# Optimization experiments

Hardware: AMD Instinct MI355X
Metric: run time of the kernel (lower is better)

Reference implementation:

```python
import jax, jax.numpy as jnp
import numpy as np

N_HEAD = 16
D_MODEL = 2048

def setup_inputs() -> dict:
    key = jax.random.key(0)
    ks = jax.random.split(key, 9)
    B, T, C = 2, 2048, D_MODEL
    s = 1.0 / np.sqrt(C)
    return {
        "idx": jax.random.normal(ks[0], (B, T, C), dtype=jnp.float32),
        "Wq": jax.random.normal(ks[1], (C, C), dtype=jnp.float32) * s,
        "bq": jnp.zeros((C,), dtype=jnp.float32),
        "Wk": jax.random.normal(ks[2], (C, C), dtype=jnp.float32) * s,
        "bk": jnp.zeros((C,), dtype=jnp.float32),
        "Wv": jax.random.normal(ks[3], (C, C), dtype=jnp.float32) * s,
        "bv": jnp.zeros((C,), dtype=jnp.float32),
        "Wo": jax.random.normal(ks[4], (C, C), dtype=jnp.float32) * s,
        "bo": jnp.zeros((C,), dtype=jnp.float32),
    }

def reference(idx, Wq, bq, Wk, bk, Wv, bv, Wo, bo):
    B, T, C = idx.shape
    hs = C // N_HEAD
    def split_heads(x):
        return x.reshape(B, T, N_HEAD, hs).transpose(0, 2, 1, 3)  # [B,H,T,hs]
    q = split_heads(idx @ Wq + bq)
    k = split_heads(idx @ Wk + bk)
    v = split_heads(idx @ Wv + bv)
    scale = 1.0 / jnp.sqrt(jnp.asarray(hs, dtype=idx.dtype))
    scores = jnp.einsum('bhqd,bhkd->bhqk', q, k) * scale
    causal = jnp.tril(jnp.ones((T, T), dtype=bool))
    scores = jnp.where(causal, scores, -jnp.inf)
    attn = jax.nn.softmax(scores, axis=-1)
    out = jnp.einsum('bhqk,bhkd->bhqd', attn, v)
    out = out.transpose(0, 2, 1, 3).reshape(B, T, C)
    return out @ Wo + bo
```

## Files before the change

### kernel.cpp

```cpp
#include <hip/hip_runtime.h>
#include <hip/hip_bf16.h>

#define TT 2048
#define CC 2048
#define HH 16
#define HS 128
#define BB 2
#define MM (BB*TT)

typedef __attribute__((ext_vector_type(8))) short bf16x8;
typedef __attribute__((ext_vector_type(4))) short bf16x4;
typedef __attribute__((ext_vector_type(4))) float f32x4;
typedef __attribute__((ext_vector_type(16))) float f32x16;

__device__ __forceinline__ short f2bf(float x) {
    unsigned u = __float_as_uint(x);
    unsigned r = (u + 0x7FFFu + ((u >> 16) & 1u)) >> 16;
    return (short)r;
}

__device__ __forceinline__ void gl_lds16(const void* g, void* l) {
    __builtin_amdgcn_global_load_lds(
        (const __attribute__((address_space(1))) unsigned int*)g,
        (__attribute__((address_space(3))) unsigned int*)l,
        16, 0, 0);
}

__global__ void cvt_bf16_kernel(const float* __restrict__ x, short* __restrict__ y, int n) {
    int stride = gridDim.x * blockDim.x;
    for (int i = blockIdx.x * blockDim.x + threadIdx.x; i < n/4; i += stride) {
        float4 v = reinterpret_cast<const float4*>(x)[i];
        bf16x4 s;
        s[0] = f2bf(v.x); s[1] = f2bf(v.y); s[2] = f2bf(v.z); s[3] = f2bf(v.w);
        reinterpret_cast<bf16x4*>(y)[i] = s;
    }
}

__global__ void wt_kernel(const float* __restrict__ w0, const float* __restrict__ w1,
                          const float* __restrict__ w2, const float* __restrict__ w3,
                          short* __restrict__ o0, short* __restrict__ o1,
                          short* __restrict__ o2, short* __restrict__ o3)
{
    const float* W; short* Wt;
    switch (blockIdx.z) {
        case 0:  W = w0; Wt = o0; break;
        case 1:  W = w1; Wt = o1; break;
        case 2:  W = w2; Wt = o2; break;
        default: W = w3; Wt = o3; break;
    }
    __shared__ float tile[32][33];
    int tx = threadIdx.x, ty = threadIdx.y;
    int k0 = blockIdx.x * 32, n0 = blockIdx.y * 32;
    #pragma unroll
    for (int i = 0; i < 4; ++i)
        tile[ty + i*8][tx] = W[(size_t)(k0 + ty + i*8) * CC + n0 + tx];
    __syncthreads();
    #pragma unroll
    for (int i = 0; i < 4; ++i)
        Wt[(size_t)(n0 + ty + i*8) * CC + k0 + tx] = f2bf(tile[tx][ty + i*8]);
}

template<int MODE>
__launch_bounds__(256)
__global__ void gemm_bt_kernel(const short* __restrict__ A, const short* __restrict__ Bt,
                               const float* __restrict__ bias, void* __restrict__ dst,
                               float scale)
{
    __shared__ __align__(16) short As[128*64];
    __shared__ __align__(16) short Bs[128*64];
    const int tid = threadIdx.x;
    const int lane = tid & 63;
    const int g = lane >> 4, fr = lane & 15;
    const int wid = tid >> 6;
    const int wr = wid >> 1, wc = wid & 1;
    const int m0 = blockIdx.x * 128, n0 = blockIdx.y * 128;

    f32x4 acc[4][4];
    #pragma unroll
    for (int i = 0; i < 4; ++i)
        #pragma unroll
        for (int j = 0; j < 4; ++j) acc[i][j] = (f32x4){0.f,0.f,0.f,0.f};

    for (int k0 = 0; k0 < CC; k0 += 64) {
        __syncthreads();
        #pragma unroll
        for (int i = 0; i < 4; ++i) {
            int c = i*256 + tid;
            int row = c >> 3;
            int kbl = ((c & 7) * 16) ^ ((row & 7) << 4);
            gl_lds16(reinterpret_cast<const char*>(A) + ((size_t)(m0+row)*CC + k0)*2 + kbl,
                     reinterpret_cast<char*>(As) + c*16);
        }
        #pragma unroll
        for (int i = 0; i < 4; ++i) {
            int c = i*256 + tid;
            int row = c >> 3;
            int kbl = ((c & 7) * 16) ^ ((row & 7) << 4);
            gl_lds16(reinterpret_cast<const char*>(Bt) + ((size_t)(n0+row)*CC + k0)*2 + kbl,
                     reinterpret_cast<char*>(Bs) + c*16);
        }
        __syncthreads();
        #pragma unroll
        for (int cch = 0; cch < 2; ++cch) {
            bf16x8 a[4], b[4];
            #pragma unroll
            for (int i = 0; i < 4; ++i) {
                int row = wr*64 + i*16 + fr;
                int kph = (cch*64 + g*16) ^ ((row & 7) << 4);
                a[i] = *reinterpret_cast<const bf16x8*>(
                    reinterpret_cast<const char*>(As) + row*128 + kph);
            }
            #pragma unroll
            for (int j = 0; j < 4; ++j) {
                int row = wc*64 + j*16 + fr;
                int kph = (cch*64 + g*16) ^ ((row & 7) << 4);
                b[j] = *reinterpret_cast<const bf16x8*>(
                    reinterpret_cast<const char*>(Bs) + row*128 + kph);
            }
            #pragma unroll
            for (int i = 0; i < 4; ++i)
                #pragma unroll
                for (int j = 0; j < 4; ++j)
                    acc[i][j] = __builtin_amdgcn_mfma_f32_16x16x32_bf16(a[i], b[j], acc[i][j], 0, 0, 0);
        }
    }

    #pragma unroll
    for (int j = 0; j < 4; ++j) {
        int n = n0 + wc*64 + j*16 + fr;
        float bv = bias[n];
        #pragma unroll
        for (int i = 0; i < 4; ++i) {
            #pragma unroll
            for (int r = 0; r < 4; ++r) {
                int m = m0 + wr*64 + i*16 + g*4 + r;
                float val = (acc[i][j][r] + bv) * scale;
                if (MODE == 0) {
                    int bb = m >> 11, t = m & (TT-1);
                    int h  = n >> 7,  d = n & (HS-1);
                    reinterpret_cast<short*>(dst)[((size_t)(bb*HH + h)*TT + t)*HS + d] = f2bf(val);
                } else if (MODE == 2) {
                    int bb = m >> 11, t = m & (TT-1);
                    int h  = n >> 7,  d = n & (HS-1);
                    reinterpret_cast<short*>(dst)[((size_t)(bb*HH + h)*HS + d)*TT + t] = f2bf(val);
                } else {
                    reinterpret_cast<float*>(dst)[(size_t)m*CC + n] = val;
                }
            }
        }
    }
}

__launch_bounds__(256, 2)
__global__ void attn_kernel(const short* __restrict__ Q, const short* __restrict__ K,
                            const short* __restrict__ Vt, short* __restrict__ O)
{
    __shared__ __align__(16) short Ks[2][64*128];
    __shared__ __align__(16) short Vs[2][128*64];

    const int tid = threadIdx.x;
    const int lane = tid & 63;
    const int wid = tid >> 6;
    const int l5 = lane >> 5;
    const int q31 = lane & 31;
    const bool hif = (l5 != 0);

    const int dd = blockIdx.x;
    const int g8 = dd & 7;
    const int s  = (dd >> 3) & 31;
    const int half = dd >> 8;
    const int bh = g8*4 + (s >> 3);
    const int u  = s & 7;
    const int qb = half ? u : (15 - u);
    const int q0 = qb * 128;
    const int wq0 = q0 + wid*32;

    const short* Qh = Q + (size_t)bh * TT * HS;
    const char*  Kg = (const char*)(K  + (size_t)bh * TT * HS);
    const char*  Vg = (const char*)(Vt + (size_t)bh * HS * TT);

    bf16x8 qf[8];
    #pragma unroll
    for (int dk = 0; dk < 8; ++dk)
        qf[dk] = *reinterpret_cast<const bf16x8*>(
            Qh + (size_t)(wq0 + q31)*HS + dk*16 + l5*8);

    f32x16 o[4];
    #pragma unroll
    for (int c = 0; c < 4; ++c)
        #pragma unroll
        for (int r = 0; r < 16; ++r) o[c][r] = 0.f;
    float mrun = -1e30f, lrun = 0.f;

    auto stage = [&](int kv0, int p) {
        char* Kd = reinterpret_cast<char*>(Ks[p]);
        char* Vd = reinterpret_cast<char*>(Vs[p]);
        #pragma unroll
        for (int i = 0; i < 4; ++i) {
            int c = i*256 + tid;
            int row = c >> 4;
            int lg  = ((c & 15) * 16) ^ ((row & 7) << 4);
            gl_lds16(Kg + (size_t)(kv0 + row)*256 + lg, Kd + c*16);
        }
        #pragma unroll
        for (int i = 0; i < 4; ++i) {
            int c = i*256 + tid;
            int row = c >> 3;
            int lg  = ((c & 7) * 16) ^ ((row & 7) << 4);
            gl_lds16(Vg + ((size_t)row*TT + kv0)*2 + lg, Vd + c*16);
        }
    };

    const int nst = q0/64 + 2;
    stage(0, 0);

    for (int t = 0; t < nst; ++t) {
        const int kv0 = t * 64;
        __syncthreads();
        if (t + 1 < nst) stage(kv0 + 64, (t+1) & 1);

        if (kv0 > wq0 + 31) continue;

        const char* Kl = reinterpret_cast<const char*>(Ks[t & 1]);
        const char* Vl = reinterpret_cast<const char*>(Vs[t & 1]);

        f32x16 st[2];
        #pragma unroll
        for (int t2 = 0; t2 < 2; ++t2)
            #pragma unroll
            for (int r = 0; r < 16; ++r) st[t2][r] = 0.f;
        #pragma unroll
        for (int t2 = 0; t2 < 2; ++t2) {
            int krow = t2*32 + q31;
            int rsw = (krow & 7) << 4;
            #pragma unroll
            for (int dk = 0; dk < 8; ++dk) {
                bf16x8 kf = *reinterpret_cast<const bf16x8*>(
                    Kl + krow*256 + ((dk*32 + l5*16) ^ rsw));
                st[t2] = __builtin_amdgcn_mfma_f32_32x32x16_bf16(kf, qf[dk], st[t2], 0, 0, 0);
            }
        }
        if (kv0 + 63 > wq0) {
            int qrow = wq0 + q31;
            #pragma unroll
            for (int t2 = 0; t2 < 2; ++t2)
                #pragma unroll
                for (int r = 0; r < 16; ++r) {
                    int kv = kv0 + t2*32 + (r & 3) + ((r >> 2) << 3) + l5*4;
                    if (kv > qrow) st[t2][r] = -1e30f;
                }
        }
        float pm = -1e30f;
        #pragma unroll
        for (int t2 = 0; t2 < 2; ++t2)
            #pragma unroll
            for (int r = 0; r < 16; ++r) pm = fmaxf(pm, st[t2][r]);
        if (__any(pm > mrun + 8.f)) {
            float pmf = fmaxf(pm, __shfl_xor(pm, 32));
            float mn = fmaxf(mrun, pmf);
            float al = __builtin_amdgcn_exp2f(mrun - mn);
            mrun = mn; lrun *= al;
            #pragma unroll
            for (int c = 0; c < 4; ++c)
                #pragma unroll
                for (int r = 0; r < 16; ++r) o[c][r] *= al;
        }
        float ps = 0.f;
        #pragma unroll
        for (int t2 = 0; t2 < 2; ++t2)
            #pragma unroll
            for (int r = 0; r < 16; ++r) {
                float pv = __builtin_amdgcn_exp2f(st[t2][r] - mrun);
                st[t2][r] = pv;
                ps += pv;
            }
        lrun += ps;
        unsigned pw[2][8];
        #pragma unroll
        for (int t2 = 0; t2 < 2; ++t2)
            #pragma unroll
            for (int w = 0; w < 8; ++w)
                asm("v_cvt_pk_bf16_f32 %0, %1, %2"
                    : "=v"(pw[t2][w]) : "v"(st[t2][2*w]), "v"(st[t2][2*w+1]));
        #pragma unroll
        for (int c4 = 0; c4 < 4; ++c4) {
            int t2 = c4 >> 1, b0 = (c4 & 1) * 4;
            unsigned A0 = pw[t2][b0+0], A1 = pw[t2][b0+1];
            unsigned A2 = pw[t2][b0+2], A3 = pw[t2][b0+3];
            unsigned X0 = (unsigned)__shfl_xor((int)A0, 32);
            unsigned X1 = (unsigned)__shfl_xor((int)A1, 32);
            unsigned X2 = (unsigned)__shfl_xor((int)A2, 32);
            unsigned X3 = (unsigned)__shfl_xor((int)A3, 32);
            union { unsigned u[4]; bf16x8 v; } fu;
            fu.u[0] = hif ? X2 : A0;
            fu.u[1] = hif ? X3 : A1;
            fu.u[2] = hif ? A2 : X0;
            fu.u[3] = hif ? A3 : X1;
            #pragma unroll
            for (int c = 0; c < 4; ++c) {
                int vrow = c*32 + q31;
                bf16x8 vf = *reinterpret_cast<const bf16x8*>(
                    Vl + vrow*128 + ((c4*32 + l5*16) ^ ((vrow & 7) << 4)));
                o[c] = __builtin_amdgcn_mfma_f32_32x32x16_bf16(vf, fu.v, o[c], 0, 0, 0);
            }
        }
    }

    lrun += __shfl_xor(lrun, 32);
    float inv = 1.f / lrun;
    int b = bh >> 4, h = bh & 15;
    size_t base = ((size_t)(b*TT + wq0 + q31))*CC + (size_t)h*HS;
    #pragma unroll
    for (int c = 0; c < 4; ++c)
        #pragma unroll
        for (int g2 = 0; g2 < 4; ++g2) {
            bf16x4 v4;
            #pragma unroll
            for (int j = 0; j < 4; ++j) v4[j] = f2bf(o[c][g2*4 + j] * inv);
            *reinterpret_cast<bf16x4*>(const_cast<short*>(O) + base + c*32 + g2*8 + l5*4) = v4;
        }
}

extern "C" void kernel_launch(void* const* d_in, const int* in_sizes, int n_in,
                              void* d_out, int out_size, void* d_ws, size_t ws_size,
                              hipStream_t stream)
{
    const float* idx = (const float*)d_in[0];
    const float* Wq  = (const float*)d_in[1];
    const float* bq  = (const float*)d_in[2];
    const float* Wk  = (const float*)d_in[3];
    const float* bk  = (const float*)d_in[4];
    const float* Wv  = (const float*)d_in[5];
    const float* bv  = (const float*)d_in[6];
    const float* Wo  = (const float*)d_in[7];
    const float* bo  = (const float*)d_in[8];
    float* out = (float*)d_out;

    short* Xbf = (short*)d_ws;
    short* Wtq = Xbf + (size_t)MM*CC;
    short* Wtk = Wtq + (size_t)CC*CC;
    short* Wtv = Wtk + (size_t)CC*CC;
    short* Wto = Wtv + (size_t)CC*CC;
    short* Qb  = Wto + (size_t)CC*CC;
    short* Kb  = Qb  + (size_t)MM*CC;
    short* Vtb = Kb  + (size_t)MM*CC;
    short* Ob  = Vtb + (size_t)MM*CC;

    cvt_bf16_kernel<<<1024, 256, 0, stream>>>(idx, Xbf, MM*CC);
    wt_kernel<<<dim3(CC/32, CC/32, 4), dim3(32, 8), 0, stream>>>(
        Wq, Wk, Wv, Wo, Wtq, Wtk, Wtv, Wto);

    const float qs = 0.08838834764831845f * 1.4426950408889634f;
    gemm_bt_kernel<0><<<dim3(MM/128, CC/128), 256, 0, stream>>>(Xbf, Wtq, bq, Qb, qs);
    gemm_bt_kernel<0><<<dim3(MM/128, CC/128), 256, 0, stream>>>(Xbf, Wtk, bk, Kb, 1.0f);
    gemm_bt_kernel<2><<<dim3(MM/128, CC/128), 256, 0, stream>>>(Xbf, Wtv, bv, Vtb, 1.0f);

    attn_kernel<<<dim3(512), 256, 0, stream>>>(Qb, Kb, Vtb, Ob);

    gemm_bt_kernel<1><<<dim3(MM/128, CC/128), 256, 0, stream>>>(Ob, Wto, bo, out, 1.0f);
}
```

Measured before the change: 262.4 us.

## Fuse Q/K/V projections into one 256x256-tiled pipelined GEMM kernel

Replaces three separate 128x128 GEMM launches for Q, K and V with one kernel over a concatenated weight matrix. It uses 256x256 tiles, 8 waves, double-buffered LDS filled by direct global-to-LDS loads with an XOR swizzle, and interleaves staging with MFMA phases under raised wave priority. A block-index swizzle groups tiles for L2 reuse. The goal is to cut launch count, raise operand reuse per LDS byte, and overlap loads with compute, at the cost of 128KB of LDS per block and a branchy scatter epilogue.

```diff
diff --git a/kernel.cpp b/kernel.cpp
--- a/kernel.cpp
+++ b/kernel.cpp
@@ -25,6 +25,14 @@
         (__attribute__((address_space(3))) unsigned int*)l,
         16, 0, 0);
 }
+
+__device__ __forceinline__ void bar() {
+    asm volatile("" ::: "memory");
+    __builtin_amdgcn_s_barrier();
+    asm volatile("" ::: "memory");
+}
+__device__ __forceinline__ void vm_wait8() { asm volatile("s_waitcnt vmcnt(8)" ::: "memory"); }
+__device__ __forceinline__ void vm_wait0() { asm volatile("s_waitcnt vmcnt(0)" ::: "memory"); }
 
 __global__ void cvt_bf16_kernel(const float* __restrict__ x, short* __restrict__ y, int n) {
     int stride = gridDim.x * blockDim.x;
@@ -60,6 +68,187 @@
         Wt[(size_t)(n0 + ty + i*8) * CC + k0 + tx] = f2bf(tile[tx][ty + i*8]);
 }
 
+__launch_bounds__(512, 2)
+__global__ void gemm_qkv_kernel(const short* __restrict__ A, const short* __restrict__ Bt,
+                                const float* __restrict__ bq, const float* __restrict__ bk,
+                                const float* __restrict__ bv,
+                                short* __restrict__ Qd, short* __restrict__ Kd,
+                                short* __restrict__ Vtd, float qscale)
+{
+    __shared__ __align__(16) short As[2][256*64];
+    __shared__ __align__(16) short Bs[2][256*64];
+
+    const int tid = threadIdx.x;
+    const int lane = tid & 63;
+    const int g = lane >> 4, fr = lane & 15;
+    const int wid = tid >> 6;
+    const int wm = wid >> 2, wn = wid & 3;
+
+    const int wg  = blockIdx.x;
+    const int swz = (wg & 7) * 48 + (wg >> 3);
+    const int m0 = (swz & 15) * 256;
+    const int n0 = (swz >> 4) * 256;
+
+    const char* Ab = (const char*)A;
+    const char* Bb = (const char*)Bt;
+
+    auto stageA = [&](int h, int tt, int b) {
+        char* dst = (char*)As[b];
+        #pragma unroll
+        for (int i = 0; i < 2; ++i) {
+            int c  = i*512 + tid;
+            int rh = c >> 3;
+            int row = (rh & 63) + h*64 + (rh >> 6)*128;
+            int kb  = (c & 7) * 16;
+            gl_lds16(Ab + ((size_t)(m0 + row)*CC + tt*64)*2 + (kb ^ ((row & 7) << 4)),
+                     dst + row*128 + kb);
+        }
+    };
+    auto stageB = [&](int nc, int tt, int b) {
+        char* dst = (char*)Bs[b];
+        #pragma unroll
+        for (int i = 0; i < 2; ++i) {
+            int c  = i*512 + tid;
+            int rb = c >> 3;
+            int row = (rb & 31) + nc*32 + (rb >> 5)*64;
+            int kb  = (c & 7) * 16;
+            gl_lds16(Bb + ((size_t)(n0 + row)*CC + tt*64)*2 + (kb ^ ((row & 7) << 4)),
+                     dst + row*128 + kb);
+        }
+    };
+
+    f32x4 acc[2][2][4][2];
+    #pragma unroll
+    for (int mr = 0; mr < 2; ++mr)
+        #pragma unroll
+        for (int nc = 0; nc < 2; ++nc)
+            #pragma unroll
+            for (int m = 0; m < 4; ++m)
+                #pragma unroll
+                for (int n = 0; n < 2; ++n)
+                    acc[mr][nc][m][n] = (f32x4){0.f,0.f,0.f,0.f};
+
+    stageA(0,0,0); stageA(1,0,0); stageB(0,0,0); stageB(1,0,0);
+    stageA(0,1,1); stageA(1,1,1); stageB(0,1,1); stageB(1,1,1);
+
+    bf16x8 a[4][2], b0[2][2], b1[2][2];
+    const int arow0 = wm*128;
+    const int brow0 = wn*64;
+
+    auto tile_body = [&](int t, int b, bool dostage) {
+        const char* Al = (const char*)As[b];
+        const char* Bl = (const char*)Bs[b];
+        bar();
+        #pragma unroll
+        for (int m = 0; m < 4; ++m)
+            #pragma unroll
+            for (int kk = 0; kk < 2; ++kk) {
+                int row = arow0 + m*16 + fr;
+                a[m][kk] = *(const bf16x8*)(Al + row*128 + ((kk*64 + g*16) ^ ((row & 7) << 4)));
+            }
+        #pragma unroll
+        for (int n = 0; n < 2; ++n)
+            #pragma unroll
+            for (int kk = 0; kk < 2; ++kk) {
+                int row = brow0 + n*16 + fr;
+                b0[n][kk] = *(const bf16x8*)(Bl + row*128 + ((kk*64 + g*16) ^ ((row & 7) << 4)));
+            }
+        __builtin_amdgcn_s_setprio(1);
+        #pragma unroll
+        for (int m = 0; m < 4; ++m)
+            #pragma unroll
+            for (int n = 0; n < 2; ++n)
+                #pragma unroll
+                for (int kk = 0; kk < 2; ++kk)
+                    acc[0][0][m][n] = __builtin_amdgcn_mfma_f32_16x16x32_bf16(a[m][kk], b0[n][kk], acc[0][0][m][n], 0, 0, 0);
+        __builtin_amdgcn_s_setprio(0);
+        bar();
+        #pragma unroll
+        for (int n = 0; n < 2; ++n)
+            #pragma unroll
+            for (int kk = 0; kk < 2; ++kk) {
+                int row = brow0 + 32 + n*16 + fr;
+                b1[n][kk] = *(const bf16x8*)(Bl + row*128 + ((kk*64 + g*16) ^ ((row & 7) << 4)));
+            }
+        if (dostage) { stageA(0, t+2, b); stageB(0, t+2, b); }
+        __builtin_amdgcn_s_setprio(1);
+        #pragma unroll
+        for (int m = 0; m < 4; ++m)
+            #pragma unroll
+            for (int n = 0; n < 2; ++n)
+                #pragma unroll
+                for (int kk = 0; kk < 2; ++kk)
+                    acc[0][1][m][n] = __builtin_amdgcn_mfma_f32_16x16x32_bf16(a[m][kk], b1[n][kk], acc[0][1][m][n], 0, 0, 0);
+        __builtin_amdgcn_s_setprio(0);
+        bar();
+        #pragma unroll
+        for (int m = 0; m < 4; ++m)
+            #pragma unroll
+            for (int kk = 0; kk < 2; ++kk) {
+                int row = arow0 + 64 + m*16 + fr;
+                a[m][kk] = *(const bf16x8*)(Al + row*128 + ((kk*64 + g*16) ^ ((row & 7) << 4)));
+            }
+        if (dostage) { stageB(1, t+2, b); }
+        __builtin_amdgcn_s_setprio(1);
+        #pragma unroll
+        for (int m = 0; m < 4; ++m)
+            #pragma unroll
+            for (int n = 0; n < 2; ++n)
+                #pragma unroll
+                for (int kk = 0; kk < 2; ++kk)
+                    acc[1][0][m][n] = __builtin_amdgcn_mfma_f32_16x16x32_bf16(a[m][kk], b0[n][kk], acc[1][0][m][n], 0, 0, 0);
+        __builtin_amdgcn_s_setprio(0);
+        bar();
+        if (dostage) { stageA(1, t+2, b); }
+        __builtin_amdgcn_s_setprio(1);
+        #pragma unroll
+        for (int m = 0; m < 4; ++m)
+            #pragma unroll
+            for (int n = 0; n < 2; ++n)
+                #pragma unroll
+                for (int kk = 0; kk < 2; ++kk)
+                    acc[1][1][m][n] = __builtin_amdgcn_mfma_f32_16x16x32_bf16(a[m][kk], b1[n][kk], acc[1][1][m][n], 0, 0, 0);
+        __builtin_amdgcn_s_setprio(0);
+    };
+
+    const int NT = CC/64;
+    #pragma unroll 1
+    for (int t = 0; t < NT-2; ++t) {
+        vm_wait8();
+        tile_body(t, t & 1, true);
+    }
+    vm_wait8();
+    tile_body(NT-2, (NT-2) & 1, false);
+    vm_wait0();
+    tile_body(NT-1, (NT-1) & 1, false);
+
+    #pragma unroll
+    for (int mr = 0; mr < 2; ++mr)
+        #pragma unroll
+        for (int nc = 0; nc < 2; ++nc)
+            #pragma unroll
+            for (int m = 0; m < 4; ++m)
+                #pragma unroll
+                for (int n = 0; n < 2; ++n) {
+                    int ng  = n0 + brow0 + nc*32 + n*16 + fr;
+                    int qkv = ng >> 11;
+                    int nn  = ng & 2047;
+                    const float* bp = (qkv == 0) ? bq : ((qkv == 1) ? bk : bv);
+                    float bval = bp[nn];
+                    float scl  = (qkv == 0) ? qscale : 1.0f;
+                    int h = nn >> 7, d = nn & (HS-1);
+                    #pragma unroll
+                    for (int r = 0; r < 4; ++r) {
+                        int mg = m0 + arow0 + mr*64 + m*16 + g*4 + r;
+                        int bb = mg >> 11, tq = mg & (TT-1);
+                        short o = f2bf((acc[mr][nc][m][n][r] + bval) * scl);
+                        if (qkv == 0)      Qd [((size_t)(bb*HH + h)*TT + tq)*HS + d] = o;
+                        else if (qkv == 1) Kd [((size_t)(bb*HH + h)*TT + tq)*HS + d] = o;
+                        else               Vtd[((size_t)(bb*HH + h)*HS + d)*TT + tq] = o;
+                    }
+                }
+}
+
 template<int MODE>
 __launch_bounds__(256)
 __global__ void gemm_bt_kernel(const short* __restrict__ A, const short* __restrict__ Bt,
@@ -135,17 +324,7 @@
             for (int r = 0; r < 4; ++r) {
                 int m = m0 + wr*64 + i*16 + g*4 + r;
                 float val = (acc[i][j][r] + bv) * scale;
-                if (MODE == 0) {
-                    int bb = m >> 11, t = m & (TT-1);
-                    int h  = n >> 7,  d = n & (HS-1);
-                    reinterpret_cast<short*>(dst)[((size_t)(bb*HH + h)*TT + t)*HS + d] = f2bf(val);
-                } else if (MODE == 2) {
-                    int bb = m >> 11, t = m & (TT-1);
-                    int h  = n >> 7,  d = n & (HS-1);
-                    reinterpret_cast<short*>(dst)[((size_t)(bb*HH + h)*HS + d)*TT + t] = f2bf(val);
-                } else {
-                    reinterpret_cast<float*>(dst)[(size_t)m*CC + n] = val;
-                }
+                reinterpret_cast<float*>(dst)[(size_t)m*CC + n] = val;
             }
         }
     }
@@ -336,24 +515,21 @@
     const float* bo  = (const float*)d_in[8];
     float* out = (float*)d_out;
 
-    short* Xbf = (short*)d_ws;
-    short* Wtq = Xbf + (size_t)MM*CC;
-    short* Wtk = Wtq + (size_t)CC*CC;
-    short* Wtv = Wtk + (size_t)CC*CC;
-    short* Wto = Wtv + (size_t)CC*CC;
-    short* Qb  = Wto + (size_t)CC*CC;
-    short* Kb  = Qb  + (size_t)MM*CC;
-    short* Vtb = Kb  + (size_t)MM*CC;
-    short* Ob  = Vtb + (size_t)MM*CC;
+    short* Xbf  = (short*)d_ws;
+    short* Wcat = Xbf  + (size_t)MM*CC;
+    short* Wto  = Wcat + (size_t)3*CC*CC;
+    short* Qb   = Wto  + (size_t)CC*CC;
+    short* Kb   = Qb   + (size_t)MM*CC;
+    short* Vtb  = Kb   + (size_t)MM*CC;
+    short* Ob   = Vtb  + (size_t)MM*CC;
 
     cvt_bf16_kernel<<<1024, 256, 0, stream>>>(idx, Xbf, MM*CC);
     wt_kernel<<<dim3(CC/32, CC/32, 4), dim3(32, 8), 0, stream>>>(
-        Wq, Wk, Wv, Wo, Wtq, Wtk, Wtv, Wto);
+        Wq, Wk, Wv, Wo,
+        Wcat, Wcat + (size_t)CC*CC, Wcat + (size_t)2*CC*CC, Wto);
 
     const float qs = 0.08838834764831845f * 1.4426950408889634f;
-    gemm_bt_kernel<0><<<dim3(MM/128, CC/128), 256, 0, stream>>>(Xbf, Wtq, bq, Qb, qs);
-    gemm_bt_kernel<0><<<dim3(MM/128, CC/128), 256, 0, stream>>>(Xbf, Wtk, bk, Kb, 1.0f);
-    gemm_bt_kernel<2><<<dim3(MM/128, CC/128), 256, 0, stream>>>(Xbf, Wtv, bv, Vtb, 1.0f);
+    gemm_qkv_kernel<<<dim3(384), 512, 0, stream>>>(Xbf, Wcat, bq, bk, bv, Qb, Kb, Vtb, qs);
 
     attn_kernel<<<dim3(512), 256, 0, stream>>>(Qb, Kb, Vtb, Ob);
 
```

Measured after the change: 309.1 us. +17.8%, slower.

## Fuse QKV projections into one GEMM launch with swizzled tile order

Applied to the files above, without the earlier changes.

Concatenates the transposed Wq/Wk/Wv into one weight buffer and runs the three projections as a single 1536-block GEMM. Each block's section decides its bias, scale and output layout. Both this kernel and the output GEMM use a 1D grid remapped by an XCD-aware swizzle, so blocks sharing A/B tiles land near each other for L2 reuse. The attention kernel also raises wave priority around its MFMA bursts. The intent is to cut launch overhead and tail effects and to improve cache locality, at the cost of a runtime branch in the epilogue.

```diff
diff --git a/kernel.cpp b/kernel.cpp
--- a/kernel.cpp
+++ b/kernel.cpp
@@ -60,11 +60,12 @@
         Wt[(size_t)(n0 + ty + i*8) * CC + k0 + tx] = f2bf(tile[tx][ty + i*8]);
 }
 
-template<int MODE>
 __launch_bounds__(256)
-__global__ void gemm_bt_kernel(const short* __restrict__ A, const short* __restrict__ Bt,
-                               const float* __restrict__ bias, void* __restrict__ dst,
-                               float scale)
+__global__ void gemm_qkv3_kernel(const short* __restrict__ A, const short* __restrict__ Wcat,
+                                 const float* __restrict__ bq, const float* __restrict__ bk,
+                                 const float* __restrict__ bv,
+                                 short* __restrict__ Qd, short* __restrict__ Kd,
+                                 short* __restrict__ Vtd, float qscale)
 {
     __shared__ __align__(16) short As[128*64];
     __shared__ __align__(16) short Bs[128*64];
@@ -73,7 +74,12 @@
     const int g = lane >> 4, fr = lane & 15;
     const int wid = tid >> 6;
     const int wr = wid >> 1, wc = wid & 1;
-    const int m0 = blockIdx.x * 128, n0 = blockIdx.y * 128;
+
+    const int bid = blockIdx.x;
+    const int swz = (bid & 7) * 192 + (bid >> 3);
+    const int m0  = (swz & 31) * 128;
+    const int nt0 = swz >> 5;
+    const short* Bt = Wcat + (size_t)nt0 * 128 * CC;
 
     f32x4 acc[4][4];
     #pragma unroll
@@ -96,7 +102,7 @@
             int c = i*256 + tid;
             int row = c >> 3;
             int kbl = ((c & 7) * 16) ^ ((row & 7) << 4);
-            gl_lds16(reinterpret_cast<const char*>(Bt) + ((size_t)(n0+row)*CC + k0)*2 + kbl,
+            gl_lds16(reinterpret_cast<const char*>(Bt) + ((size_t)row*CC + k0)*2 + kbl,
                      reinterpret_cast<char*>(Bs) + c*16);
         }
         __syncthreads();
@@ -125,29 +131,107 @@
         }
     }
 
+    const int sec = nt0 >> 4;
+    const float scl = (sec == 0) ? qscale : 1.0f;
+    const float* bp = (sec == 0) ? bq : ((sec == 1) ? bk : bv);
+    #pragma unroll
+    for (int j = 0; j < 4; ++j) {
+        int nn = (nt0 & 15)*128 + wc*64 + j*16 + fr;
+        float bval = bp[nn];
+        int h = nn >> 7, d = nn & (HS-1);
+        #pragma unroll
+        for (int i = 0; i < 4; ++i) {
+            #pragma unroll
+            for (int r = 0; r < 4; ++r) {
+                int mg = m0 + wr*64 + i*16 + g*4 + r;
+                int bb = mg >> 11, tq = mg & (TT-1);
+                short ov = f2bf((acc[i][j][r] + bval) * scl);
+                if (sec == 0)      Qd [((size_t)(bb*HH + h)*TT + tq)*HS + d] = ov;
+                else if (sec == 1) Kd [((size_t)(bb*HH + h)*TT + tq)*HS + d] = ov;
+                else               Vtd[((size_t)(bb*HH + h)*HS + d)*TT + tq] = ov;
+            }
+        }
+    }
+}
+
+__launch_bounds__(256)
+__global__ void gemm_out_kernel(const short* __restrict__ A, const short* __restrict__ Bt,
+                                const float* __restrict__ bias, float* __restrict__ dst)
+{
+    __shared__ __align__(16) short As[128*64];
+    __shared__ __align__(16) short Bs[128*64];
+    const int tid = threadIdx.x;
+    const int lane = tid & 63;
+    const int g = lane >> 4, fr = lane & 15;
+    const int wid = tid >> 6;
+    const int wr = wid >> 1, wc = wid & 1;
+
+    const int bid = blockIdx.x;
+    const int swz = (bid & 7) * 64 + (bid >> 3);
+    const int m0 = (swz & 31) * 128;
+    const int n0 = (swz >> 5) * 128;
+
+    f32x4 acc[4][4];
+    #pragma unroll
+    for (int i = 0; i < 4; ++i)
+        #pragma unroll
+        for (int j = 0; j < 4; ++j) acc[i][j] = (f32x4){0.f,0.f,0.f,0.f};
+
+    for (int k0 = 0; k0 < CC; k0 += 64) {
+        __syncthreads();
+        #pragma unroll
+        for (int i = 0; i < 4; ++i) {
+            int c = i*256 + tid;
+            int row = c >> 3;
+            int kbl = ((c & 7) * 16) ^ ((row & 7) << 4);
+            gl_lds16(reinterpret_cast<const char*>(A) + ((size_t)(m0+row)*CC + k0)*2 + kbl,
+                     reinterpret_cast<char*>(As) + c*16);
+        }
+        #pragma unroll
+        for (int i = 0; i < 4; ++i) {
+            int c = i*256 + tid;
+            int row = c >> 3;
+            int kbl = ((c & 7) * 16) ^ ((row & 7) << 4);
+            gl_lds16(reinterpret_cast<const char*>(Bt) + ((size_t)(n0+row)*CC + k0)*2 + kbl,
+                     reinterpret_cast<char*>(Bs) + c*16);
+        }
+        __syncthreads();
+        #pragma unroll
+        for (int cch = 0; cch < 2; ++cch) {
+            bf16x8 a[4], b[4];
+            #pragma unroll
+            for (int i = 0; i < 4; ++i) {
+                int row = wr*64 + i*16 + fr;
+                int kph = (cch*64 + g*16) ^ ((row & 7) << 4);
+                a[i] = *reinterpret_cast<const bf16x8*>(
+                    reinterpret_cast<const char*>(As) + row*128 + kph);
+            }
+            #pragma unroll
+            for (int j = 0; j < 4; ++j) {
+                int row = wc*64 + j*16 + fr;
+                int kph = (cch*64 + g*16) ^ ((row & 7) << 4);
+                b[j] = *reinterpret_cast<const bf16x8*>(
+                    reinterpret_cast<const char*>(Bs) + row*128 + kph);
+            }
+            #pragma unroll
+            for (int i = 0; i < 4; ++i)
+                #pragma unroll
+                for (int j = 0; j < 4; ++j)
+                    acc[i][j] = __builtin_amdgcn_mfma_f32_16x16x32_bf16(a[i], b[j], acc[i][j], 0, 0, 0);
+        }
+    }
+
     #pragma unroll
     for (int j = 0; j < 4; ++j) {
         int n = n0 + wc*64 + j*16 + fr;
-        float bv = bias[n];
-        #pragma unroll
-        for (int i = 0; i < 4; ++i) {
+        float bval = bias[n];
+        #pragma unroll
+        for (int i = 0; i < 4; ++i)
             #pragma unroll
             for (int r = 0; r < 4; ++r) {
                 int m = m0 + wr*64 + i*16 + g*4 + r;
-                float val = (acc[i][j][r] + bv) * scale;
-                if (MODE == 0) {
-                    int bb = m >> 11, t = m & (TT-1);
-                    int h  = n >> 7,  d = n & (HS-1);
-                    reinterpret_cast<short*>(dst)[((size_t)(bb*HH + h)*TT + t)*HS + d] = f2bf(val);
-                } else if (MODE == 2) {
-                    int bb = m >> 11, t = m & (TT-1);
-                    int h  = n >> 7,  d = n & (HS-1);
-                    reinterpret_cast<short*>(dst)[((size_t)(bb*HH + h)*HS + d)*TT + t] = f2bf(val);
-                } else {
-                    reinterpret_cast<float*>(dst)[(size_t)m*CC + n] = val;
-                }
-            }
-        }
+                dst[(size_t)m*CC + n] = acc[i][j][r] + bval;
+            }
     }
 }
 
@@ -229,6 +313,7 @@
         for (int t2 = 0; t2 < 2; ++t2)
             #pragma unroll
             for (int r = 0; r < 16; ++r) st[t2][r] = 0.f;
+        __builtin_amdgcn_s_setprio(1);
         #pragma unroll
         for (int t2 = 0; t2 < 2; ++t2) {
             int krow = t2*32 + q31;
@@ -240,6 +325,7 @@
                 st[t2] = __builtin_amdgcn_mfma_f32_32x32x16_bf16(kf, qf[dk], st[t2], 0, 0, 0);
             }
         }
+        __builtin_amdgcn_s_setprio(0);
         if (kv0 + 63 > wq0) {
             int qrow = wq0 + q31;
             #pragma unroll
@@ -296,6 +382,7 @@
             fu.u[1] = hif ? X3 : A1;
             fu.u[2] = hif ? A2 : X0;
             fu.u[3] = hif ? A3 : X1;
+            __builtin_amdgcn_s_setprio(1);
             #pragma unroll
             for (int c = 0; c < 4; ++c) {
                 int vrow = c*32 + q31;
@@ -303,6 +390,7 @@
                     Vl + vrow*128 + ((c4*32 + l5*16) ^ ((vrow & 7) << 4)));
                 o[c] = __builtin_amdgcn_mfma_f32_32x32x16_bf16(vf, fu.v, o[c], 0, 0, 0);
             }
+            __builtin_amdgcn_s_setprio(0);
         }
     }
 
@@ -317,7 +405,7 @@
             bf16x4 v4;
             #pragma unroll
             for (int j = 0; j < 4; ++j) v4[j] = f2bf(o[c][g2*4 + j] * inv);
-            *reinterpret_cast<bf16x4*>(const_cast<short*>(O) + base + c*32 + g2*8 + l5*4) = v4;
+            *reinterpret_cast<bf16x4*>(O + base + c*32 + g2*8 + l5*4) = v4;
         }
 }
 
@@ -336,26 +424,23 @@
     const float* bo  = (const float*)d_in[8];
     float* out = (float*)d_out;
 
-    short* Xbf = (short*)d_ws;
-    short* Wtq = Xbf + (size_t)MM*CC;
-    short* Wtk = Wtq + (size_t)CC*CC;
-    short* Wtv = Wtk + (size_t)CC*CC;
-    short* Wto = Wtv + (size_t)CC*CC;
-    short* Qb  = Wto + (size_t)CC*CC;
-    short* Kb  = Qb  + (size_t)MM*CC;
-    short* Vtb = Kb  + (size_t)MM*CC;
-    short* Ob  = Vtb + (size_t)MM*CC;
+    short* Xbf  = (short*)d_ws;
+    short* Wcat = Xbf  + (size_t)MM*CC;
+    short* Wto  = Wcat + (size_t)3*CC*CC;
+    short* Qb   = Wto  + (size_t)CC*CC;
+    short* Kb   = Qb   + (size_t)MM*CC;
+    short* Vtb  = Kb   + (size_t)MM*CC;
+    short* Ob   = Vtb  + (size_t)MM*CC;
 
     cvt_bf16_kernel<<<1024, 256, 0, stream>>>(idx, Xbf, MM*CC);
     wt_kernel<<<dim3(CC/32, CC/32, 4), dim3(32, 8), 0, stream>>>(
-        Wq, Wk, Wv, Wo, Wtq, Wtk, Wtv, Wto);
+        Wq, Wk, Wv, Wo,
+        Wcat, Wcat + (size_t)CC*CC, Wcat + (size_t)2*CC*CC, Wto);
 
     const float qs = 0.08838834764831845f * 1.4426950408889634f;
-    gemm_bt_kernel<0><<<dim3(MM/128, CC/128), 256, 0, stream>>>(Xbf, Wtq, bq, Qb, qs);
-    gemm_bt_kernel<0><<<dim3(MM/128, CC/128), 256, 0, stream>>>(Xbf, Wtk, bk, Kb, 1.0f);
-    gemm_bt_kernel<2><<<dim3(MM/128, CC/128), 256, 0, stream>>>(Xbf, Wtv, bv, Vtb, 1.0f);
+    gemm_qkv3_kernel<<<dim3(1536), 256, 0, stream>>>(Xbf, Wcat, bq, bk, bv, Qb, Kb, Vtb, qs);
 
     attn_kernel<<<dim3(512), 256, 0, stream>>>(Qb, Kb, Vtb, Ob);
 
-    gemm_bt_kernel<1><<<dim3(MM/128, CC/128), 256, 0, stream>>>(Ob, Wto, bo, out, 1.0f);
-}
+    gemm_out_kernel<<<dim3(512), 256, 0, stream>>>(Ob, Wto, bo, out);
+}
```

After: 308.0 us. 17.4% more time.

## Pair causal query tiles per block for balanced attention work with 2-wave blocks

Applied to the files above, without the earlier changes.

The attention kernel now launches 128-thread blocks that each process two 64-row query tiles, a late tile (31-p) and an early tile (p), over a combined 33 KV steps. This gives every block the same amount of causal work instead of the previous 128-row tiles with uneven lengths. The output flush moves into a lambda that runs when the block switches tiles. s_setprio hints are also added around the MFMA sections to favour matrix issue. The trade-off is that each block has half as many waves to hide latency, and with launch bounds changed to (128,1) the per-SM occupancy may drop.

```diff
diff --git a/kernel.cpp b/kernel.cpp
--- a/kernel.cpp
+++ b/kernel.cpp
@@ -151,7 +151,7 @@
     }
 }
 
-__launch_bounds__(256, 2)
+__launch_bounds__(128, 1)
 __global__ void attn_kernel(const short* __restrict__ Q, const short* __restrict__ K,
                             const short* __restrict__ Vt, short* __restrict__ O)
 {
@@ -167,18 +167,18 @@
 
     const int dd = blockIdx.x;
     const int g8 = dd & 7;
-    const int s  = (dd >> 3) & 31;
-    const int half = dd >> 8;
-    const int bh = g8*4 + (s >> 3);
-    const int u  = s & 7;
-    const int qb = half ? u : (15 - u);
-    const int q0 = qb * 128;
-    const int wq0 = q0 + wid*32;
+    const int i0 = dd >> 3;
+    const int bh = g8*4 + (i0 >> 4);
+    const int p  = i0 & 15;
+    const int nstA = 32 - p;
+    const int ntot = 33;
 
     const short* Qh = Q + (size_t)bh * TT * HS;
     const char*  Kg = (const char*)(K  + (size_t)bh * TT * HS);
     const char*  Vg = (const char*)(Vt + (size_t)bh * HS * TT);
 
+    int wq0 = (31 - p)*64 + wid*32;
+
     bf16x8 qf[8];
     #pragma unroll
     for (int dk = 0; dk < 8; ++dk)
@@ -192,34 +192,65 @@
         for (int r = 0; r < 16; ++r) o[c][r] = 0.f;
     float mrun = -1e30f, lrun = 0.f;
 
-    auto stage = [&](int kv0, int p) {
-        char* Kd = reinterpret_cast<char*>(Ks[p]);
-        char* Vd = reinterpret_cast<char*>(Vs[p]);
-        #pragma unroll
-        for (int i = 0; i < 4; ++i) {
-            int c = i*256 + tid;
+    auto stage = [&](int kv0, int pb) {
+        char* Kd = reinterpret_cast<char*>(Ks[pb]);
+        char* Vd = reinterpret_cast<char*>(Vs[pb]);
+        #pragma unroll
+        for (int i = 0; i < 8; ++i) {
+            int c = i*128 + tid;
             int row = c >> 4;
             int lg  = ((c & 15) * 16) ^ ((row & 7) << 4);
             gl_lds16(Kg + (size_t)(kv0 + row)*256 + lg, Kd + c*16);
         }
         #pragma unroll
-        for (int i = 0; i < 4; ++i) {
-            int c = i*256 + tid;
+        for (int i = 0; i < 8; ++i) {
+            int c = i*128 + tid;
             int row = c >> 3;
             int lg  = ((c & 7) * 16) ^ ((row & 7) << 4);
             gl_lds16(Vg + ((size_t)row*TT + kv0)*2 + lg, Vd + c*16);
         }
     };
 
-    const int nst = q0/64 + 2;
+    auto flush = [&]() {
+        float lr = lrun + __shfl_xor(lrun, 32);
+        float inv = 1.f / lr;
+        int b = bh >> 4, h = bh & 15;
+        size_t base = ((size_t)(b*TT + wq0 + q31))*CC + (size_t)h*HS;
+        #pragma unroll
+        for (int c = 0; c < 4; ++c)
+            #pragma unroll
+            for (int g2 = 0; g2 < 4; ++g2) {
+                bf16x4 v4;
+                #pragma unroll
+                for (int j = 0; j < 4; ++j) v4[j] = f2bf(o[c][g2*4 + j] * inv);
+                *reinterpret_cast<bf16x4*>(O + base + c*32 + g2*8 + l5*4) = v4;
+            }
+    };
+
     stage(0, 0);
 
-    for (int t = 0; t < nst; ++t) {
-        const int kv0 = t * 64;
+    #pragma unroll 1
+    for (int t = 0; t < ntot; ++t) {
+        const int kv0 = ((t >= nstA) ? t - nstA : t) * 64;
         __syncthreads();
-        if (t + 1 < nst) stage(kv0 + 64, (t+1) & 1);
-
-        if (kv0 > wq0 + 31) continue;
+        if (t + 1 < ntot) {
+            int tn = t + 1;
+            int kvn = ((tn >= nstA) ? tn - nstA : tn) * 64;
+            stage(kvn, tn & 1);
+        }
+        if (t == nstA) {
+            flush();
+            wq0 = p*64 + wid*32;
+            #pragma unroll
+            for (int dk = 0; dk < 8; ++dk)
+                qf[dk] = *reinterpret_cast<const bf16x8*>(
+                    Qh + (size_t)(wq0 + q31)*HS + dk*16 + l5*8);
+            #pragma unroll
+            for (int c = 0; c < 4; ++c)
+                #pragma unroll
+                for (int r = 0; r < 16; ++r) o[c][r] = 0.f;
+            mrun = -1e30f; lrun = 0.f;
+        }
 
         const char* Kl = reinterpret_cast<const char*>(Ks[t & 1]);
         const char* Vl = reinterpret_cast<const char*>(Vs[t & 1]);
@@ -229,6 +260,7 @@
         for (int t2 = 0; t2 < 2; ++t2)
             #pragma unroll
             for (int r = 0; r < 16; ++r) st[t2][r] = 0.f;
+        __builtin_amdgcn_s_setprio(1);
         #pragma unroll
         for (int t2 = 0; t2 < 2; ++t2) {
             int krow = t2*32 + q31;
@@ -240,6 +272,7 @@
                 st[t2] = __builtin_amdgcn_mfma_f32_32x32x16_bf16(kf, qf[dk], st[t2], 0, 0, 0);
             }
         }
+        __builtin_amdgcn_s_setprio(0);
         if (kv0 + 63 > wq0) {
             int qrow = wq0 + q31;
             #pragma unroll
@@ -296,6 +329,7 @@
             fu.u[1] = hif ? X3 : A1;
             fu.u[2] = hif ? A2 : X0;
             fu.u[3] = hif ? A3 : X1;
+            __builtin_amdgcn_s_setprio(1);
             #pragma unroll
             for (int c = 0; c < 4; ++c) {
                 int vrow = c*32 + q31;
@@ -303,22 +337,11 @@
                     Vl + vrow*128 + ((c4*32 + l5*16) ^ ((vrow & 7) << 4)));
                 o[c] = __builtin_amdgcn_mfma_f32_32x32x16_bf16(vf, fu.v, o[c], 0, 0, 0);
             }
-        }
-    }
-
-    lrun += __shfl_xor(lrun, 32);
-    float inv = 1.f / lrun;
-    int b = bh >> 4, h = bh & 15;
-    size_t base = ((size_t)(b*TT + wq0 + q31))*CC + (size_t)h*HS;
-    #pragma unroll
-    for (int c = 0; c < 4; ++c)
-        #pragma unroll
-        for (int g2 = 0; g2 < 4; ++g2) {
-            bf16x4 v4;
-            #pragma unroll
-            for (int j = 0; j < 4; ++j) v4[j] = f2bf(o[c][g2*4 + j] * inv);
-            *reinterpret_cast<bf16x4*>(const_cast<short*>(O) + base + c*32 + g2*8 + l5*4) = v4;
-        }
+            __builtin_amdgcn_s_setprio(0);
+        }
+    }
+
+    flush();
 }
 
 extern "C" void kernel_launch(void* const* d_in, const int* in_sizes, int n_in,
@@ -355,7 +378,7 @@
     gemm_bt_kernel<0><<<dim3(MM/128, CC/128), 256, 0, stream>>>(Xbf, Wtk, bk, Kb, 1.0f);
     gemm_bt_kernel<2><<<dim3(MM/128, CC/128), 256, 0, stream>>>(Xbf, Wtv, bv, Vtb, 1.0f);
 
-    attn_kernel<<<dim3(512), 256, 0, stream>>>(Qb, Kb, Vtb, Ob);
+    attn_kernel<<<dim3(512), 128, 0, stream>>>(Qb, Kb, Vtb, Ob);
 
     gemm_bt_kernel<1><<<dim3(MM/128, CC/128), 256, 0, stream>>>(Ob, Wto, bo, out, 1.0f);
 }
```

Result: slower. 283.3 us (+8.0%).
